# Kernel tuning notes

Hardware: AMD Instinct MI355X
Metric: run time of the kernel (lower is better)

## Reference

```python
import jax, jax.numpy as jnp
import numpy as np

PLANE_SIZE = 512
N_LEVELS = 8
FEATURE_DIM = 16
N_PTS = 524288


def setup_inputs() -> dict:
    key = jax.random.key(0)
    k1, k2, k3 = jax.random.split(key, 3)
    x = jax.random.uniform(k1, (N_PTS, 3), dtype=jnp.float32)
    # per-point float mip level bias in [0, n_levels-1]
    level = jax.random.uniform(k2, (N_PTS, 1), dtype=jnp.float32) * (N_LEVELS - 1)
    fm = jax.random.uniform(k3, (3, PLANE_SIZE, PLANE_SIZE, FEATURE_DIM),
                            minval=-0.01, maxval=0.01, dtype=jnp.float32)
    return {"x": x, "level": level, "fm": fm, "n_levels": N_LEVELS}


def _bilinear(flat_pyr, offsets, sizes, uv, lvl_i):
    # flat_pyr: (3, T, C) concatenated mip levels; uv: (3, N, 2); lvl_i: (3, N) int32
    size = sizes[lvl_i]                      # (3, N) texture size at this mip
    fsize = size.astype(uv.dtype)
    px = uv[..., 0] * fsize - 0.5            # u -> width axis (nvdiffrast convention)
    py = uv[..., 1] * fsize - 0.5            # v -> height axis
    x0 = jnp.floor(px)
    y0 = jnp.floor(py)
    fx = (px - x0)[..., None]
    fy = (py - y0)[..., None]
    x0i = x0.astype(jnp.int32)
    y0i = y0.astype(jnp.int32)
    xa = jnp.clip(x0i, 0, size - 1)          # boundary_mode='clamp'
    xb = jnp.clip(x0i + 1, 0, size - 1)
    ya = jnp.clip(y0i, 0, size - 1)
    yb = jnp.clip(y0i + 1, 0, size - 1)
    base = offsets[lvl_i]
    p = jnp.arange(3)[:, None]
    g = lambda yy, xx: flat_pyr[p, base + yy * size + xx]   # (3, N, C) gather
    f00 = g(ya, xa); f01 = g(ya, xb); f10 = g(yb, xa); f11 = g(yb, xb)
    return (f00 * (1 - fx) + f01 * fx) * (1 - fy) + (f10 * (1 - fx) + f11 * fx) * fy


def reference(x, level, fm, n_levels):
    N = x.shape[0]
    C = fm.shape[-1]
    # build mip pyramid via 2x2 box filter (nvdiffrast auto-mips)
    levels = [fm]
    for _ in range(n_levels - 1):
        t = levels[-1]
        s = t.shape[1]
        levels.append(t.reshape(3, s // 2, 2, s // 2, 2, C).mean(axis=(2, 4)))
    sizes_list = [l.shape[1] for l in levels]
    offsets = jnp.asarray(np.cumsum([0] + [s * s for s in sizes_list[:-1]]), jnp.int32)
    sizes = jnp.asarray(sizes_list, jnp.int32)
    flat_pyr = jnp.concatenate([l.reshape(3, -1, C) for l in levels], axis=1)  # (3, T, C)
    # tri-plane decomposition: plane0 sees (y,z), plane1 (x,z), plane2 (x,y)
    uv = jnp.stack([x[:, [1, 2]], x[:, [0, 2]], x[:, [0, 1]]], axis=0)  # (3, N, 2)
    max_mip = n_levels - 1
    lvl = jnp.clip(jnp.broadcast_to(level.reshape(1, N), (3, N)), 0.0, float(max_mip))
    l0 = jnp.floor(lvl)
    f = (lvl - l0)[..., None]                # (3, N, 1) level fraction
    l0i = l0.astype(jnp.int32)
    l1i = jnp.minimum(l0i + 1, max_mip)
    s0 = _bilinear(flat_pyr, offsets, sizes, uv, l0i)
    s1 = _bilinear(flat_pyr, offsets, sizes, uv, l1i)
    enc = s0 * (1 - f) + s1 * f              # (3, N, C) trilinear (mip-lerped)
    # permute(1,2,0,3).view(N, 3C): per point, concat plane0|plane1|plane2 features
    return jnp.transpose(enc, (1, 0, 2)).reshape(N, 3 * C)
```

## Files before the change

kernel.cpp:

```cpp
#include <hip/hip_runtime.h>
#include <hip/hip_fp16.h>


typedef float        f4v   __attribute__((ext_vector_type(4)));
typedef unsigned int u32x2 __attribute__((ext_vector_type(2)));
typedef unsigned int u32x4 __attribute__((ext_vector_type(4)));

#define FM_PLANE_STRIDE (262144 * 16)
#define WS_PLANE_STRIDE (87376 * 16)
#define PSTRIDE_H (349520 * 16)
#define WS_H_BYTES (3ull * PSTRIDE_H * 2ull)
#define LVL4_OFF 348160u

__device__ __forceinline__ unsigned lvl_off(int l) {
    return (1048576u - (1048576u >> (2 * l))) / 3u;
}

__device__ __forceinline__ f4v ld4(const float* p) {
    return *reinterpret_cast<const f4v*>(p);
}
__device__ __forceinline__ f4v ld4nt(const float* p) {
    return __builtin_nontemporal_load(reinterpret_cast<const f4v*>(p));
}
__device__ __forceinline__ void st4(float* p, f4v v) {
    *reinterpret_cast<f4v*>(p) = v;
}
__device__ __forceinline__ void st4nt(float* p, f4v v) {
    __builtin_nontemporal_store(v, reinterpret_cast<f4v*>(p));
}
__device__ __forceinline__ f4v ldraw_h(const __half* p) {
    return *reinterpret_cast<const f4v*>(p);
}
__device__ __forceinline__ u32x2 pack4(f4v v) {
    __half2 lo = __floats2half2_rn(v.x, v.y);
    __half2 hi = __floats2half2_rn(v.z, v.w);
    u32x2 r;
    r.x = *reinterpret_cast<unsigned*>(&lo);
    r.y = *reinterpret_cast<unsigned*>(&hi);
    return r;
}
__device__ __forceinline__ f4v h4f(const __half* p) {
    u32x2 u = *reinterpret_cast<const u32x2*>(p);
    unsigned a0 = u.x, a1 = u.y;
    __half2 lo = *reinterpret_cast<__half2*>(&a0);
    __half2 hi = *reinterpret_cast<__half2*>(&a1);
    float2 flo = __half22float2(lo), fhi = __half22float2(hi);
    f4v r; r.x = flo.x; r.y = flo.y; r.z = fhi.x; r.w = fhi.y;
    return r;
}
__device__ __forceinline__ float2 up2(float rawcomp) {
    unsigned u = __float_as_uint(rawcomp);
    __half2 hh = *reinterpret_cast<__half2*>(&u);
    return __half22float2(hh);
}


__global__ __launch_bounds__(1024) void mip_build_all(
    const float* __restrict__ fm, __half* __restrict__ wsh)
{
    __shared__ f4v A[32 * 32 * 4];
    __shared__ f4v B[16 * 16 * 4];

    const int tile = blockIdx.x;
    const int p    = blockIdx.y;
    const int ty = tile >> 3, tx = tile & 7;
    const int tid = threadIdx.x;
    const int q = tid & 3;

    __half* plane = wsh + (size_t)p * PSTRIDE_H;
    __half* L1 = plane + (size_t)lvl_off(1) * 16;
    __half* L2 = plane + (size_t)lvl_off(2) * 16;
    __half* L3 = plane + (size_t)lvl_off(3) * 16;
    __half* L4 = plane + (size_t)lvl_off(4) * 16;
    __half* L5 = plane + (size_t)lvl_off(5) * 16;
    __half* L6 = plane + (size_t)lvl_off(6) * 16;
    const float* fp = fm + (size_t)p * FM_PLANE_STRIDE;

    #pragma unroll
    for (int k = 0; k < 4; ++k) {
        int s = (tid + k * 1024) >> 2;
        int ly = s >> 5, lx = s & 31;
        int gy = ty * 32 + ly, gx = tx * 32 + lx;
        const float* sp = fp + ((size_t)(2 * gy) * 512 + 2 * gx) * 16 + q * 4;
        f4v r = (ld4nt(sp) + ld4nt(sp + 16) +
                 ld4nt(sp + 512 * 16) + ld4nt(sp + 512 * 16 + 16)) * 0.25f;
        A[s * 4 + q] = r;
        *reinterpret_cast<u32x2*>(L1 + ((size_t)gy * 256 + gx) * 16 + q * 4) = pack4(r);
    }
    __syncthreads();

    {
        int s = tid >> 2;
        int ly = s >> 4, lx = s & 15;
        f4v r = (A[((2 * ly) * 32 + 2 * lx) * 4 + q]     + A[((2 * ly) * 32 + 2 * lx + 1) * 4 + q] +
                 A[((2 * ly + 1) * 32 + 2 * lx) * 4 + q] + A[((2 * ly + 1) * 32 + 2 * lx + 1) * 4 + q]) * 0.25f;
        B[s * 4 + q] = r;
        *reinterpret_cast<u32x2*>(L2 + ((size_t)(ty * 16 + ly) * 128 + tx * 16 + lx) * 16 + q * 4) = pack4(r);
    }
    __syncthreads();

    if (tid < 256) {
        int s = tid >> 2;
        int ly = s >> 3, lx = s & 7;
        f4v r = (B[((2 * ly) * 16 + 2 * lx) * 4 + q]     + B[((2 * ly) * 16 + 2 * lx + 1) * 4 + q] +
                 B[((2 * ly + 1) * 16 + 2 * lx) * 4 + q] + B[((2 * ly + 1) * 16 + 2 * lx + 1) * 4 + q]) * 0.25f;
        A[s * 4 + q] = r;
        *reinterpret_cast<u32x2*>(L3 + ((size_t)(ty * 8 + ly) * 64 + tx * 8 + lx) * 16 + q * 4) = pack4(r);
    }
    __syncthreads();

    if (tid < 64) {
        int s = tid >> 2;
        int ly = s >> 2, lx = s & 3;
        f4v r = (A[((2 * ly) * 8 + 2 * lx) * 4 + q]     + A[((2 * ly) * 8 + 2 * lx + 1) * 4 + q] +
                 A[((2 * ly + 1) * 8 + 2 * lx) * 4 + q] + A[((2 * ly + 1) * 8 + 2 * lx + 1) * 4 + q]) * 0.25f;
        B[s * 4 + q] = r;
        *reinterpret_cast<u32x2*>(L4 + ((size_t)(ty * 4 + ly) * 32 + tx * 4 + lx) * 16 + q * 4) = pack4(r);
    }
    __syncthreads();

    if (tid < 16) {
        int s = tid >> 2;
        int ly = s >> 1, lx = s & 1;
        f4v r = (B[((2 * ly) * 4 + 2 * lx) * 4 + q]     + B[((2 * ly) * 4 + 2 * lx + 1) * 4 + q] +
                 B[((2 * ly + 1) * 4 + 2 * lx) * 4 + q] + B[((2 * ly + 1) * 4 + 2 * lx + 1) * 4 + q]) * 0.25f;
        A[s * 4 + q] = r;
        *reinterpret_cast<u32x2*>(L5 + ((size_t)(ty * 2 + ly) * 16 + tx * 2 + lx) * 16 + q * 4) = pack4(r);
    }
    __syncthreads();

    if (tid < 4) {
        f4v r = (A[0 * 4 + q] + A[1 * 4 + q] + A[2 * 4 + q] + A[3 * 4 + q]) * 0.25f;
        *reinterpret_cast<u32x2*>(L6 + ((size_t)(ty * 8 + tx)) * 16 + q * 4) = pack4(r);
    }
}

__device__ __forceinline__ void bilerp8_h(
    const __half* __restrict__ wplane, const __half* __restrict__ lds_h,
    int l, float u, float v, int h, float* o)
{
    const int sz = 512 >> l;
    const float fsz = (float)sz;
    float px = u * fsz - 0.5f;
    float py = v * fsz - 0.5f;
    float xf = floorf(px), yf = floorf(py);
    float fx = px - xf, fy = py - yf;
    int xi = (int)xf, yi = (int)yf;
    int xa = min(max(xi, 0), sz - 1);
    int xb = min(xi + 1, sz - 1);
    int ya = min(max(yi, 0), sz - 1);
    int yb = min(yi + 1, sz - 1);
    f4v q00, q01, q10, q11;
    if (l >= 4) {
        const __half* base = lds_h + (size_t)(lvl_off(l) - LVL4_OFF) * 16 + h * 8;
        const __half* r0 = base + (ya * sz) * 16;
        const __half* r1 = base + (yb * sz) * 16;
        q00 = ldraw_h(r0 + xa * 16);
        q01 = ldraw_h(r0 + xb * 16);
        q10 = ldraw_h(r1 + xa * 16);
        q11 = ldraw_h(r1 + xb * 16);
    } else {
        const __half* base = wplane + (size_t)lvl_off(l) * 16 + h * 8;
        const __half* r0 = base + (size_t)(ya * sz) * 16;
        const __half* r1 = base + (size_t)(yb * sz) * 16;
        q00 = ldraw_h(r0 + (size_t)xa * 16);
        q01 = ldraw_h(r0 + (size_t)xb * 16);
        q10 = ldraw_h(r1 + (size_t)xa * 16);
        q11 = ldraw_h(r1 + (size_t)xb * 16);
    }
    float gx = 1.f - fx, gy = 1.f - fy;
    float w00 = gx * gy, w01 = fx * gy, w10 = gx * fy, w11 = fx * fy;
    #pragma unroll
    for (int i = 0; i < 4; ++i) {
        float2 a = up2(q00[i]), b = up2(q01[i]), c = up2(q10[i]), d = up2(q11[i]);
        o[2 * i]     = a.x * w00 + b.x * w01 + c.x * w10 + d.x * w11;
        o[2 * i + 1] = a.y * w00 + b.y * w01 + c.y * w10 + d.y * w11;
    }
}

__device__ __forceinline__ void bilerp8_f0(
    const float* __restrict__ fmp, float u, float v, int h, float* o)
{
    float px = u * 512.f - 0.5f;
    float py = v * 512.f - 0.5f;
    float xf = floorf(px), yf = floorf(py);
    float fx = px - xf, fy = py - yf;
    int xi = (int)xf, yi = (int)yf;
    int xa = min(max(xi, 0), 511);
    int xb = min(xi + 1, 511);
    int ya = min(max(yi, 0), 511);
    int yb = min(yi + 1, 511);
    const float* r0 = fmp + (size_t)(ya * 512) * 16 + h * 8;
    const float* r1 = fmp + (size_t)(yb * 512) * 16 + h * 8;
    f4v p00a = ld4(r0 + (size_t)xa * 16), p00b = ld4(r0 + (size_t)xa * 16 + 4);
    f4v p01a = ld4(r0 + (size_t)xb * 16), p01b = ld4(r0 + (size_t)xb * 16 + 4);
    f4v p10a = ld4(r1 + (size_t)xa * 16), p10b = ld4(r1 + (size_t)xa * 16 + 4);
    f4v p11a = ld4(r1 + (size_t)xb * 16), p11b = ld4(r1 + (size_t)xb * 16 + 4);
    float gx = 1.f - fx, gy = 1.f - fy;
    float w00 = gx * gy, w01 = fx * gy, w10 = gx * fy, w11 = fx * fy;
    #pragma unroll
    for (int i = 0; i < 4; ++i) {
        o[i]     = p00a[i] * w00 + p01a[i] * w01 + p10a[i] * w10 + p11a[i] * w11;
        o[4 + i] = p00b[i] * w00 + p01b[i] * w01 + p10b[i] * w10 + p11b[i] * w11;
    }
}

__global__ __launch_bounds__(1024) void trimip_sample_h(
    const float* __restrict__ xyz, const float* __restrict__ level,
    const float* __restrict__ fm, const __half* __restrict__ wsh,
    float* __restrict__ out, int N)
{
    __shared__ u32x4 lds[2720];
    const int p = blockIdx.y;
    const __half* wplane = wsh + (size_t)p * PSTRIDE_H;
    for (int uidx = threadIdx.x; uidx < 2688; uidx += 1024) {
        lds[uidx] = *reinterpret_cast<const u32x4*>(
            wplane + (size_t)LVL4_OFF * 16 + (size_t)uidx * 8);
    }
    __syncthreads();
    __half* lds_h = reinterpret_cast<__half*>(lds);

    if (threadIdx.x < 64) {
        int q = threadIdx.x & 3, i = threadIdx.x >> 2;
        int y = i >> 2, x = i & 3;
        f4v r = (h4f(lds_h + (size_t)(1280 + (2 * y) * 8 + 2 * x) * 16 + q * 4) +
                 h4f(lds_h + (size_t)(1280 + (2 * y) * 8 + 2 * x + 1) * 16 + q * 4) +
                 h4f(lds_h + (size_t)(1280 + (2 * y + 1) * 8 + 2 * x) * 16 + q * 4) +
                 h4f(lds_h + (size_t)(1280 + (2 * y + 1) * 8 + 2 * x + 1) * 16 + q * 4)) * 0.25f;
        *reinterpret_cast<u32x2*>(lds_h + (size_t)(1344 + i) * 16 + q * 4) = pack4(r);
    }
    __syncthreads();

    const int n = blockIdx.x * 512 + (threadIdx.x >> 1);
    if (n >= N) return;
    const int h = threadIdx.x & 1;

    const float c0 = xyz[n * 3 + 0];
    const float c1 = xyz[n * 3 + 1];
    const float c2 = xyz[n * 3 + 2];
    const float u = (p == 0) ? c1 : c0;
    const float v = (p == 2) ? c1 : c2;

    float lv = level[n];
    lv = fminf(fmaxf(lv, 0.f), 7.f);
    float lf = floorf(lv);
    float f = lv - lf;
    int l0 = (int)lf;
    int l1 = min(l0 + 1, 7);

    float s0[8], s1[8];
    if (l0 == 0) {
        bilerp8_f0(fm + (size_t)p * FM_PLANE_STRIDE, u, v, h, s0);
    } else {
        bilerp8_h(wplane, lds_h, l0, u, v, h, s0);
    }
    bilerp8_h(wplane, lds_h, l1, u, v, h, s1);

    float g = 1.f - f;
    f4v oa, ob;
    #pragma unroll
    for (int i = 0; i < 4; ++i) {
        oa[i] = s0[i] * g + s1[i] * f;
        ob[i] = s0[4 + i] * g + s1[4 + i] * f;
    }
    float* op = out + (size_t)((n * 3 + p) * 2 + h) * 8;
    st4nt(op, oa);
    st4nt(op + 4, ob);
}


__device__ __forceinline__ f4v avg4(f4v a, f4v b, f4v c, f4v d) {
    return (a + b + c + d) * 0.25f;
}

__global__ __launch_bounds__(256) void mip_build_f(
    const float* __restrict__ src, float* __restrict__ dst)
{
    int t = blockIdx.x * blockDim.x + threadIdx.x;
    const int p = blockIdx.y;
    const int q = t & 3, idx = t >> 2;
    const int y = idx >> 8, x = idx & 255;
    const float* sp = src + (size_t)p * FM_PLANE_STRIDE
                          + ((size_t)(2 * y) * 512 + 2 * x) * 16 + q * 4;
    f4v r = avg4(ld4(sp), ld4(sp + 16), ld4(sp + 512 * 16), ld4(sp + 512 * 16 + 16));
    st4(dst + (size_t)p * WS_PLANE_STRIDE + ((size_t)y * 256 + x) * 16 + q * 4, r);
}

__global__ __launch_bounds__(256) void mip_tail_f(float* __restrict__ mips)
{
    const int tile = blockIdx.x, q = blockIdx.y, p = blockIdx.z;
    const int ty = tile >> 2, tx = tile & 3;
    const int tid = threadIdx.x;
    __shared__ f4v A[32 * 32];
    __shared__ f4v B[16 * 16];
    float* plane = mips + (size_t)p * WS_PLANE_STRIDE;
    const float* L1 = plane;
    float* L2 = plane + (size_t)65536 * 16;
    float* L3 = plane + (size_t)81920 * 16;
    float* L4 = plane + (size_t)86016 * 16;
    float* L5 = plane + (size_t)87040 * 16;
    float* L6 = plane + (size_t)87296 * 16;
    float* L7 = plane + (size_t)87360 * 16;

    #pragma unroll
    for (int k = 0; k < 4; ++k) {
        int li = tid + k * 256;
        int ly = li >> 5, lx = li & 31;
        int gy = ty * 32 + ly, gx = tx * 32 + lx;
        const float* sp = L1 + ((size_t)(2 * gy) * 256 + 2 * gx) * 16 + q * 4;
        f4v r = avg4(ld4(sp), ld4(sp + 16), ld4(sp + 256 * 16), ld4(sp + 256 * 16 + 16));
        A[li] = r;
        st4(L2 + ((size_t)gy * 128 + gx) * 16 + q * 4, r);
    }
    __syncthreads();
    {
        int ly = tid >> 4, lx = tid & 15;
        f4v r = avg4(A[(2 * ly) * 32 + 2 * lx],     A[(2 * ly) * 32 + 2 * lx + 1],
                     A[(2 * ly + 1) * 32 + 2 * lx], A[(2 * ly + 1) * 32 + 2 * lx + 1]);
        B[tid] = r;
        st4(L3 + ((size_t)(ty * 16 + ly) * 64 + tx * 16 + lx) * 16 + q * 4, r);
    }
    __syncthreads();
    if (tid < 64) {
        int ly = tid >> 3, lx = tid & 7;
        f4v r = avg4(B[(2 * ly) * 16 + 2 * lx],     B[(2 * ly) * 16 + 2 * lx + 1],
                     B[(2 * ly + 1) * 16 + 2 * lx], B[(2 * ly + 1) * 16 + 2 * lx + 1]);
        A[tid] = r;
        st4(L4 + ((size_t)(ty * 8 + ly) * 32 + tx * 8 + lx) * 16 + q * 4, r);
    }
    __syncthreads();
    if (tid < 16) {
        int ly = tid >> 2, lx = tid & 3;
        f4v r = avg4(A[(2 * ly) * 8 + 2 * lx],     A[(2 * ly) * 8 + 2 * lx + 1],
                     A[(2 * ly + 1) * 8 + 2 * lx], A[(2 * ly + 1) * 8 + 2 * lx + 1]);
        B[tid] = r;
        st4(L5 + ((size_t)(ty * 4 + ly) * 16 + tx * 4 + lx) * 16 + q * 4, r);
    }
    __syncthreads();
    if (tid < 4) {
        int ly = tid >> 1, lx = tid & 1;
        f4v r = avg4(B[(2 * ly) * 4 + 2 * lx],     B[(2 * ly) * 4 + 2 * lx + 1],
                     B[(2 * ly + 1) * 4 + 2 * lx], B[(2 * ly + 1) * 4 + 2 * lx + 1]);
        A[tid] = r;
        st4(L6 + ((size_t)(ty * 2 + ly) * 8 + tx * 2 + lx) * 16 + q * 4, r);
    }
    __syncthreads();
    if (tid == 0) {
        f4v r = avg4(A[0], A[1], A[2], A[3]);
        st4(L7 + ((size_t)ty * 4 + tx) * 16 + q * 4, r);
    }
}

__device__ __forceinline__ f4v bilerp_f(
    const float* __restrict__ fm, const float* __restrict__ mips,
    int p, int l, float u, float v, int q)
{
    const int sz = 512 >> l;
    const float fsz = (float)sz;
    float px = u * fsz - 0.5f;
    float py = v * fsz - 0.5f;
    float xf = floorf(px), yf = floorf(py);
    float fx = px - xf, fy = py - yf;
    int xi = (int)xf, yi = (int)yf;
    int xa = min(max(xi, 0), sz - 1);
    int xb = min(xi + 1, sz - 1);
    int ya = min(max(yi, 0), sz - 1);
    int yb = min(yi + 1, sz - 1);
    const float* base;
    if (l == 0) {
        base = fm + (size_t)p * FM_PLANE_STRIDE;
    } else {
        unsigned off = (262144u - ((unsigned)(sz * sz) << 2)) / 3u;
        base = mips + (size_t)p * WS_PLANE_STRIDE + (size_t)off * 16;
    }
    const float* r0 = base + (size_t)(ya * sz) * 16 + q * 4;
    const float* r1 = base + (size_t)(yb * sz) * 16 + q * 4;
    f4v f00 = ld4(r0 + xa * 16);
    f4v f01 = ld4(r0 + xb * 16);
    f4v f10 = ld4(r1 + xa * 16);
    f4v f11 = ld4(r1 + xb * 16);
    float gx = 1.f - fx, gy = 1.f - fy;
    return (f00 * gx + f01 * fx) * gy + (f10 * gx + f11 * fx) * fy;
}

__global__ __launch_bounds__(256) void trimip_sample_f(
    const float* __restrict__ xyz, const float* __restrict__ level,
    const float* __restrict__ fm, const float* __restrict__ mips,
    float* __restrict__ out, int N)
{
    int t = blockIdx.x * blockDim.x + threadIdx.x;
    if (t >= N * 12) return;
    const int q = t & 3;
    const int r = t >> 2;
    const int n = r / 3;
    const int p = r - n * 3;
    const float c0 = xyz[n * 3 + 0];
    const float c1 = xyz[n * 3 + 1];
    const float c2 = xyz[n * 3 + 2];
    const float u = (p == 0) ? c1 : c0;
    const float v = (p == 2) ? c1 : c2;
    float lv = level[n];
    lv = fminf(fmaxf(lv, 0.f), 7.f);
    float lf = floorf(lv);
    float f = lv - lf;
    int l0 = (int)lf;
    int l1 = min(l0 + 1, 7);
    f4v s0 = bilerp_f(fm, mips, p, l0, u, v, q);
    f4v s1 = bilerp_f(fm, mips, p, l1, u, v, q);
    f4v o = s0 * (1.f - f) + s1 * f;
    st4nt(out + (size_t)t * 4, o);
}

extern "C" void kernel_launch(void* const* d_in, const int* in_sizes, int n_in,
                              void* d_out, int out_size, void* d_ws, size_t ws_size,
                              hipStream_t stream) {
    const float* xyz   = (const float*)d_in[0];
    const float* level = (const float*)d_in[1];
    const float* fm    = (const float*)d_in[2];
    float* out = (float*)d_out;
    const int N = in_sizes[1];

    if (ws_size >= WS_H_BYTES) {
        __half* wsh = (__half*)d_ws;
        mip_build_all<<<dim3(64, 3), 1024, 0, stream>>>(fm, wsh);
        trimip_sample_h<<<dim3((N + 511) / 512, 3), 1024, 0, stream>>>(
            xyz, level, fm, wsh, out, N);
    } else {
        float* mips = (float*)d_ws;
        mip_build_f<<<dim3(1024, 3), dim3(256), 0, stream>>>(fm, mips);
        mip_tail_f<<<dim3(16, 4, 3), dim3(256), 0, stream>>>(mips);
        const int total = N * 12;
        trimip_sample_f<<<(total + 255) / 256, 256, 0, stream>>>(xyz, level, fm, mips, out, N);
    }
}
```

Measured before the change: 216.0 us.

## Store level-0 as fp16 in workspace and issue both mip taps before blending

The mip builder now also writes a half-precision copy of the base level into the workspace, so the sampler reads every level, level 0 included, from fp16 data instead of the fp32 feature map. The sampler issues all eight texel loads for both mip levels before doing any interpolation, which removes the branch on level 0 and lets the loads overlap. This halves the bytes fetched for level-0 taps, at the cost of writing an extra 24 MB fp16 plane set and some fp16 rounding error at level 0.

```diff
diff --git a/kernel.cpp b/kernel.cpp
--- a/kernel.cpp
+++ b/kernel.cpp
@@ -68,6 +68,7 @@
     const int q = tid & 3;
 
     __half* plane = wsh + (size_t)p * PSTRIDE_H;
+    __half* L0 = plane;
     __half* L1 = plane + (size_t)lvl_off(1) * 16;
     __half* L2 = plane + (size_t)lvl_off(2) * 16;
     __half* L3 = plane + (size_t)lvl_off(3) * 16;
@@ -82,8 +83,16 @@
         int ly = s >> 5, lx = s & 31;
         int gy = ty * 32 + ly, gx = tx * 32 + lx;
         const float* sp = fp + ((size_t)(2 * gy) * 512 + 2 * gx) * 16 + q * 4;
-        f4v r = (ld4nt(sp) + ld4nt(sp + 16) +
-                 ld4nt(sp + 512 * 16) + ld4nt(sp + 512 * 16 + 16)) * 0.25f;
+        f4v a = ld4nt(sp);
+        f4v b = ld4nt(sp + 16);
+        f4v c = ld4nt(sp + 512 * 16);
+        f4v d = ld4nt(sp + 512 * 16 + 16);
+        size_t o00 = ((size_t)(2 * gy) * 512 + 2 * gx) * 16 + q * 4;
+        *reinterpret_cast<u32x2*>(L0 + o00)                 = pack4(a);
+        *reinterpret_cast<u32x2*>(L0 + o00 + 16)            = pack4(b);
+        *reinterpret_cast<u32x2*>(L0 + o00 + 512 * 16)      = pack4(c);
+        *reinterpret_cast<u32x2*>(L0 + o00 + 512 * 16 + 16) = pack4(d);
+        f4v r = (a + b + c + d) * 0.25f;
         A[s * 4 + q] = r;
         *reinterpret_cast<u32x2*>(L1 + ((size_t)gy * 256 + gx) * 16 + q * 4) = pack4(r);
     }
@@ -135,22 +144,23 @@
     }
 }
 
-__device__ __forceinline__ void bilerp8_h(
+__device__ __forceinline__ void tap_issue(
     const __half* __restrict__ wplane, const __half* __restrict__ lds_h,
-    int l, float u, float v, int h, float* o)
+    int l, float u, float v, int h,
+    f4v& q00, f4v& q01, f4v& q10, f4v& q11, float& fx, float& fy)
 {
     const int sz = 512 >> l;
     const float fsz = (float)sz;
     float px = u * fsz - 0.5f;
     float py = v * fsz - 0.5f;
     float xf = floorf(px), yf = floorf(py);
-    float fx = px - xf, fy = py - yf;
+    fx = px - xf;
+    fy = py - yf;
     int xi = (int)xf, yi = (int)yf;
     int xa = min(max(xi, 0), sz - 1);
     int xb = min(xi + 1, sz - 1);
     int ya = min(max(yi, 0), sz - 1);
     int yb = min(yi + 1, sz - 1);
-    f4v q00, q01, q10, q11;
     if (l >= 4) {
         const __half* base = lds_h + (size_t)(lvl_off(l) - LVL4_OFF) * 16 + h * 8;
         const __half* r0 = base + (ya * sz) * 16;
@@ -168,47 +178,11 @@
         q10 = ldraw_h(r1 + (size_t)xa * 16);
         q11 = ldraw_h(r1 + (size_t)xb * 16);
     }
-    float gx = 1.f - fx, gy = 1.f - fy;
-    float w00 = gx * gy, w01 = fx * gy, w10 = gx * fy, w11 = fx * fy;
-    #pragma unroll
-    for (int i = 0; i < 4; ++i) {
-        float2 a = up2(q00[i]), b = up2(q01[i]), c = up2(q10[i]), d = up2(q11[i]);
-        o[2 * i]     = a.x * w00 + b.x * w01 + c.x * w10 + d.x * w11;
-        o[2 * i + 1] = a.y * w00 + b.y * w01 + c.y * w10 + d.y * w11;
-    }
-}
-
-__device__ __forceinline__ void bilerp8_f0(
-    const float* __restrict__ fmp, float u, float v, int h, float* o)
-{
-    float px = u * 512.f - 0.5f;
-    float py = v * 512.f - 0.5f;
-    float xf = floorf(px), yf = floorf(py);
-    float fx = px - xf, fy = py - yf;
-    int xi = (int)xf, yi = (int)yf;
-    int xa = min(max(xi, 0), 511);
-    int xb = min(xi + 1, 511);
-    int ya = min(max(yi, 0), 511);
-    int yb = min(yi + 1, 511);
-    const float* r0 = fmp + (size_t)(ya * 512) * 16 + h * 8;
-    const float* r1 = fmp + (size_t)(yb * 512) * 16 + h * 8;
-    f4v p00a = ld4(r0 + (size_t)xa * 16), p00b = ld4(r0 + (size_t)xa * 16 + 4);
-    f4v p01a = ld4(r0 + (size_t)xb * 16), p01b = ld4(r0 + (size_t)xb * 16 + 4);
-    f4v p10a = ld4(r1 + (size_t)xa * 16), p10b = ld4(r1 + (size_t)xa * 16 + 4);
-    f4v p11a = ld4(r1 + (size_t)xb * 16), p11b = ld4(r1 + (size_t)xb * 16 + 4);
-    float gx = 1.f - fx, gy = 1.f - fy;
-    float w00 = gx * gy, w01 = fx * gy, w10 = gx * fy, w11 = fx * fy;
-    #pragma unroll
-    for (int i = 0; i < 4; ++i) {
-        o[i]     = p00a[i] * w00 + p01a[i] * w01 + p10a[i] * w10 + p11a[i] * w11;
-        o[4 + i] = p00b[i] * w00 + p01b[i] * w01 + p10b[i] * w10 + p11b[i] * w11;
-    }
 }
 
 __global__ __launch_bounds__(1024) void trimip_sample_h(
     const float* __restrict__ xyz, const float* __restrict__ level,
-    const float* __restrict__ fm, const __half* __restrict__ wsh,
-    float* __restrict__ out, int N)
+    const __half* __restrict__ wsh, float* __restrict__ out, int N)
 {
     __shared__ u32x4 lds[2720];
     const int p = blockIdx.y;
@@ -248,13 +222,32 @@
     int l0 = (int)lf;
     int l1 = min(l0 + 1, 7);
 
+    f4v a00, a01, a10, a11, b00, b01, b10, b11;
+    float fx0, fy0, fx1, fy1;
+    tap_issue(wplane, lds_h, l0, u, v, h, a00, a01, a10, a11, fx0, fy0);
+    tap_issue(wplane, lds_h, l1, u, v, h, b00, b01, b10, b11, fx1, fy1);
+
     float s0[8], s1[8];
-    if (l0 == 0) {
-        bilerp8_f0(fm + (size_t)p * FM_PLANE_STRIDE, u, v, h, s0);
-    } else {
-        bilerp8_h(wplane, lds_h, l0, u, v, h, s0);
-    }
-    bilerp8_h(wplane, lds_h, l1, u, v, h, s1);
+    {
+        float gx = 1.f - fx0, gy = 1.f - fy0;
+        float w00 = gx * gy, w01 = fx0 * gy, w10 = gx * fy0, w11 = fx0 * fy0;
+        #pragma unroll
+        for (int i = 0; i < 4; ++i) {
+            float2 a = up2(a00[i]), b = up2(a01[i]), c = up2(a10[i]), d = up2(a11[i]);
+            s0[2 * i]     = a.x * w00 + b.x * w01 + c.x * w10 + d.x * w11;
+            s0[2 * i + 1] = a.y * w00 + b.y * w01 + c.y * w10 + d.y * w11;
+        }
+    }
+    {
+        float gx = 1.f - fx1, gy = 1.f - fy1;
+        float w00 = gx * gy, w01 = fx1 * gy, w10 = gx * fy1, w11 = fx1 * fy1;
+        #pragma unroll
+        for (int i = 0; i < 4; ++i) {
+            float2 a = up2(b00[i]), b = up2(b01[i]), c = up2(b10[i]), d = up2(b11[i]);
+            s1[2 * i]     = a.x * w00 + b.x * w01 + c.x * w10 + d.x * w11;
+            s1[2 * i + 1] = a.y * w00 + b.y * w01 + c.y * w10 + d.y * w11;
+        }
+    }
 
     float g = 1.f - f;
     f4v oa, ob;
@@ -424,7 +417,7 @@
         __half* wsh = (__half*)d_ws;
         mip_build_all<<<dim3(64, 3), 1024, 0, stream>>>(fm, wsh);
         trimip_sample_h<<<dim3((N + 511) / 512, 3), 1024, 0, stream>>>(
-            xyz, level, fm, wsh, out, N);
+            xyz, level, wsh, out, N);
     } else {
         float* mips = (float*)d_ws;
         mip_build_f<<<dim3(1024, 3), dim3(256), 0, stream>>>(fm, mips);
```

Result: faster. 194.1 us (-10.1%).
